# Kernel tuning notes

Hardware: AMD Instinct MI355X
Metric: run time of the kernel (lower is better)

The kernel has to match this reference:

```python
import jax, jax.numpy as jnp
import numpy as np

B, S, H = 2, 2048, 2048
NH, HD = 16, 128


def rotate_half(x):
    x1, x2 = x[..., : x.shape[-1] // 2], x[..., x.shape[-1] // 2 :]
    return jnp.concatenate((-x2, x1), axis=-1)


def setup_inputs() -> dict:
    key = jax.random.key(0)
    ks = jax.random.split(key, 8)
    return {
        "hidden": jax.random.normal(ks[0], (B, S, H), dtype=jnp.float32),
        "cos": jax.random.uniform(ks[1], (S, HD), dtype=jnp.float32),
        "sin": jax.random.uniform(ks[2], (S, HD), dtype=jnp.float32),
        "attention_mask": jnp.zeros((B, 1, S, S), dtype=jnp.float32),
        "Wq": jax.random.normal(ks[3], (H, H), dtype=jnp.float32) * 0.02,
        "Wk": jax.random.normal(ks[4], (H, H), dtype=jnp.float32) * 0.02,
        "Wv": jax.random.normal(ks[5], (H, H), dtype=jnp.float32) * 0.02,
        "Wo": jax.random.normal(ks[6], (H, H), dtype=jnp.float32) * 0.02,
    }


def reference(hidden, cos, sin, attention_mask, Wq, Wk, Wv, Wo):
    b, s, h = hidden.shape
    # torch Linear: y = x @ W.T ; reshape to [B, NH, S, HD]
    def proj(W):
        return (hidden @ W.T).reshape(b, s, NH, HD).transpose(0, 2, 1, 3)

    q, k, v = proj(Wq), proj(Wk), proj(Wv)
    c = cos[None, None, :, :]  # [1,1,S,HD]
    si = sin[None, None, :, :]
    q = q * c + rotate_half(q) * si
    k = k * c + rotate_half(k) * si
    scores = jnp.einsum("bhqd,bhkd->bhqk", q, k) / jnp.sqrt(jnp.float32(HD))
    scores = scores + attention_mask
    attn = jax.nn.softmax(scores.astype(jnp.float32), axis=-1).astype(q.dtype)
    out = jnp.einsum("bhqk,bhkd->bhqd", attn, v)
    out = out.transpose(0, 2, 1, 3).reshape(b, s, h)
    return out @ Wo.T
```

## Files before the change

### kernel.cpp

```cpp
#include <hip/hip_runtime.h>
#include <hip/hip_bf16.h>
#include <math.h>

#define SEQ 2048
#define HID 2048
#define NHEAD 16
#define HDIM 128
#define LDQ 6144

typedef __bf16 bf16_t;
typedef __bf16 bf16x2 __attribute__((ext_vector_type(2)));
typedef __bf16 bf16x4_t __attribute__((ext_vector_type(4)));
typedef __bf16 bf16x8 __attribute__((ext_vector_type(8)));
typedef float f32x4 __attribute__((ext_vector_type(4)));
typedef float f32x16 __attribute__((ext_vector_type(16)));
typedef unsigned u32x4 __attribute__((ext_vector_type(4)));

#define MFMA16(a, b, c) __builtin_amdgcn_mfma_f32_16x16x32_bf16(a, b, c, 0, 0, 0)
#define MFMA32(a, b, c) __builtin_amdgcn_mfma_f32_32x32x16_bf16(a, b, c, 0, 0, 0)
#define GLOAD_LDS(g, l) \
  __builtin_amdgcn_global_load_lds((const __attribute__((address_space(1))) void*)(g), \
                                   (__attribute__((address_space(3))) void*)(l), 16, 0, 0)

static __device__ inline unsigned pk2(float lo, float hi) {
  bf16x2 t; t[0] = (bf16_t)lo; t[1] = (bf16_t)hi;
  return __builtin_bit_cast(unsigned, t);
}

__global__ void cast_hidden(const float* __restrict__ in, bf16_t* __restrict__ out) {
  int i = blockIdx.x * 256 + threadIdx.x;
  float4 v = ((const float4*)in)[i];
  bf16x4_t b;
  b[0] = (bf16_t)v.x; b[1] = (bf16_t)v.y; b[2] = (bf16_t)v.z; b[3] = (bf16_t)v.w;
  ((bf16x4_t*)out)[i] = b;
}

__global__ void cast_weights(const float* __restrict__ a, const float* __restrict__ b,
                             const float* __restrict__ c, const float* __restrict__ d,
                             bf16_t* __restrict__ out) {
  const float* srcs[4] = {a, b, c, d};
  const float* src = srcs[blockIdx.y];
  bf16_t* dst = out + (size_t)blockIdx.y * (HID * HID);
  int i = blockIdx.x * 256 + threadIdx.x;
  float4 v = ((const float4*)src)[i];
  bf16x4_t o;
  o[0] = (bf16_t)v.x; o[1] = (bf16_t)v.y; o[2] = (bf16_t)v.z; o[3] = (bf16_t)v.w;
  ((bf16x4_t*)dst)[i] = o;
}

__global__ __launch_bounds__(512, 2) void gemm256(
    const bf16_t* __restrict__ A, const bf16_t* __restrict__ Bw,
    bf16_t* __restrict__ Cb, float* __restrict__ Cf, int M, int N, int K) {
  __shared__ char smem[131072];
  const int tid = threadIdx.x, lane = tid & 63, wid = tid >> 6;
  const int wr = wid >> 2, wc = wid & 3;
  const int lr = lane & 15, lg = lane >> 4;
  const int xcd = blockIdx.x & 7, l = blockIdx.x >> 3;
  const int brow = (xcd >> 2) * 8 + l / 6;
  const int bcol = (xcd & 3) * 6 + l % 6;
  const int NT = K >> 6;

  const bf16_t* Ab = A + (size_t)(brow * 256) * K;
  const bf16_t* Bb = Bw + (size_t)(bcol * 256) * K;

  f32x4 acc[8][4] = {};
  bf16x8 af[4], bfr[4];
  const int swz = (lg ^ ((lr >> 1) & 3)) << 4;

#define STAGE_HALF(t_, op, kh)                                                        \
  {                                                                                   \
    int tt = (t_) < NT ? (t_) : NT - 1;                                               \
    const bf16_t* gsrc = (op) ? Bb : Ab;                                              \
    char* ldst = smem + (tt & 1) * 65536 + (op) * 32768 + (kh) * 16384;               \
    _Pragma("unroll") for (int is = 0; is < 2; ++is) {                                \
      int p = tid + is * 512;                                                         \
      int row = p >> 2, ch = p & 3;                                                   \
      GLOAD_LDS(gsrc + (size_t)row * K + tt * 64 + (kh) * 32 +                        \
                    ((ch ^ ((row >> 1) & 3)) * 8),                                    \
                ldst + p * 16);                                                       \
    }                                                                                 \
  }

#define PHASE(cb, kh, mh, LOADB, STAGECALL, VM)                                       \
  {                                                                                   \
    _Pragma("unroll") for (int mf = 0; mf < 4; ++mf) {                                \
      int row = wr * 128 + (mh) * 64 + mf * 16 + lr;                                  \
      af[mf] = *(const bf16x8*)(smem + (cb) * 65536 + (kh) * 16384 + row * 64 + swz); \
    }                                                                                 \
    if (LOADB) {                                                                      \
      _Pragma("unroll") for (int nf = 0; nf < 4; ++nf) {                              \
        int row = wc * 64 + nf * 16 + lr;                                             \
        bfr[nf] = *(const bf16x8*)(smem + (cb) * 65536 + 32768 + (kh) * 16384 +       \
                                   row * 64 + swz);                                   \
      }                                                                               \
    }                                                                                 \
    STAGECALL;                                                                        \
    __builtin_amdgcn_s_barrier();                                                     \
    asm volatile("s_waitcnt lgkmcnt(0)" ::: "memory");                                \
    __builtin_amdgcn_sched_barrier(0);                                                \
    __builtin_amdgcn_s_setprio(1);                                                    \
    _Pragma("unroll") for (int mf = 0; mf < 4; ++mf)                                  \
      _Pragma("unroll") for (int nf = 0; nf < 4; ++nf)                                \
        acc[(mh) * 4 + mf][nf] = MFMA16(af[mf], bfr[nf], acc[(mh) * 4 + mf][nf]);     \
    __builtin_amdgcn_s_setprio(0);                                                    \
    if (VM) { asm volatile("s_waitcnt vmcnt(6)" ::: "memory"); }                      \
    __builtin_amdgcn_s_barrier();                                                     \
    __builtin_amdgcn_sched_barrier(0);                                                \
  }

  STAGE_HALF(0, 1, 0); STAGE_HALF(0, 0, 0); STAGE_HALF(0, 1, 1); STAGE_HALF(0, 0, 1);
  STAGE_HALF(1, 1, 0); STAGE_HALF(1, 0, 0); STAGE_HALF(1, 1, 1);
  asm volatile("s_waitcnt vmcnt(6)" ::: "memory");
  __builtin_amdgcn_s_barrier();
  __builtin_amdgcn_sched_barrier(0);

  const int NI = NT >> 1;
  for (int i = 0; i < NI; ++i) {
    const int t2 = 2 * i;
    PHASE(0, 0, 0, 1, STAGE_HALF(t2 + 1, 0, 1), 0);
    PHASE(0, 0, 1, 0, STAGE_HALF(t2 + 2, 1, 0), 0);
    PHASE(0, 1, 0, 1, STAGE_HALF(t2 + 2, 0, 0), 0);
    PHASE(0, 1, 1, 0, STAGE_HALF(t2 + 2, 1, 1), 1);
    PHASE(1, 0, 0, 1, STAGE_HALF(t2 + 2, 0, 1), 0);
    PHASE(1, 0, 1, 0, STAGE_HALF(t2 + 3, 1, 0), 0);
    PHASE(1, 1, 0, 1, STAGE_HALF(t2 + 3, 0, 0), 0);
    PHASE(1, 1, 1, 0, STAGE_HALF(t2 + 3, 1, 1), 1);
  }
#undef PHASE
#undef STAGE_HALF

#pragma unroll
  for (int mi = 0; mi < 8; ++mi)
#pragma unroll
    for (int nf = 0; nf < 4; ++nf)
#pragma unroll
      for (int r = 0; r < 4; ++r) {
        int row = brow * 256 + wr * 128 + (mi >> 2) * 64 + (mi & 3) * 16 + lg * 4 + r;
        int col = bcol * 256 + wc * 64 + nf * 16 + lr;
        float v = acc[mi][nf][r];
        if (Cf) Cf[(size_t)row * N + col] = v;
        else    Cb[(size_t)row * N + col] = (bf16_t)v;
      }
}

__global__ __launch_bounds__(256, 3) void gemm_bt(
    const bf16_t* __restrict__ A, const bf16_t* __restrict__ Bw,
    bf16_t* __restrict__ Cb, float* __restrict__ Cf,
    int M, int N, int K) {
  __shared__ bf16_t As[2][128 * 32];
  __shared__ bf16_t Bs[2][128 * 32];
  const int tid = threadIdx.x;
  const int lane = tid & 63, wid = tid >> 6;
  const int wr = wid >> 1, wc = wid & 1;
  const int lr = lane & 15, lg = lane >> 4;
  const int nwg = gridDim.x;
  const int lid = (blockIdx.x & 7) * (nwg >> 3) + (blockIdx.x >> 3);
  const int nbc = N >> 7;
  const int brow = lid / nbc, bcol = lid % nbc;

  f32x4 acc[4][4] = {};
  const int swz = lg ^ ((lr >> 1) & 3);

  const int srow = tid >> 2, sch = tid & 3;
#define GSTAGE(k0, bb)                                                                   \
  {                                                                                      \
    _Pragma("unroll") for (int is = 0; is < 2; ++is) {                                   \
      int row = srow + is * 64;                                                          \
      int g = (sch ^ ((row >> 1) & 3)) * 8;                                              \
      GLOAD_LDS(A + (size_t)(brow * 128 + row) * K + (k0) + g,                           \
                &As[bb][(row * 4 + sch) * 8]);                                           \
      GLOAD_LDS(Bw + (size_t)(bcol * 128 + row) * K + (k0) + g,                          \
                &Bs[bb][(row * 4 + sch) * 8]);                                           \
    }                                                                                    \
  }

  GSTAGE(0, 0);
  __syncthreads();

  const int nt = K / 32;
  for (int t = 0; t < nt; ++t) {
    const int cb = t & 1;
    if (t + 1 < nt) GSTAGE((t + 1) * 32, cb ^ 1);
    bf16x8 af[4], bfr[4];
#pragma unroll
    for (int m = 0; m < 4; ++m)
      af[m] = *(const bf16x8*)(&As[cb][(wr * 64 + m * 16 + lr) * 32 + swz * 8]);
#pragma unroll
    for (int n = 0; n < 4; ++n)
      bfr[n] = *(const bf16x8*)(&Bs[cb][(wc * 64 + n * 16 + lr) * 32 + swz * 8]);
#pragma unroll
    for (int m = 0; m < 4; ++m)
#pragma unroll
      for (int n = 0; n < 4; ++n)
        acc[m][n] = MFMA16(af[m], bfr[n], acc[m][n]);
    __syncthreads();
  }
#undef GSTAGE

#pragma unroll
  for (int m = 0; m < 4; ++m)
#pragma unroll
    for (int n = 0; n < 4; ++n)
#pragma unroll
      for (int r = 0; r < 4; ++r) {
        int row = brow * 128 + wr * 64 + m * 16 + lg * 4 + r;
        int col = bcol * 128 + wc * 64 + n * 16 + lr;
        float v = acc[m][n][r];
        if (Cf) Cf[(size_t)row * N + col] = v;
        else    Cb[(size_t)row * N + col] = (bf16_t)v;
      }
}

__global__ void rope_qk(bf16_t* __restrict__ QKV,
                        const float* __restrict__ cost, const float* __restrict__ sint) {
  const float SCALE = 0.08838834764831845f;
  int idx = blockIdx.x * 256 + threadIdx.x;
  int d8 = idx & 7;
  int t = idx >> 3;
  int h = t & 15;
  int row = t >> 4;
  int s = row & (SEQ - 1);
  size_t base = (size_t)row * LDQ + h * HDIM;
  const float4* cp = (const float4*)(cost + s * HDIM);
  const float4* sp = (const float4*)(sint + s * HDIM);
  float4 c0a = cp[d8 * 2], c0b = cp[d8 * 2 + 1];
  float4 c1a = cp[16 + d8 * 2], c1b = cp[16 + d8 * 2 + 1];
  float4 s0a = sp[d8 * 2], s0b = sp[d8 * 2 + 1];
  float4 s1a = sp[16 + d8 * 2], s1b = sp[16 + d8 * 2 + 1];
  float c0[8] = {c0a.x, c0a.y, c0a.z, c0a.w, c0b.x, c0b.y, c0b.z, c0b.w};
  float c1[8] = {c1a.x, c1a.y, c1a.z, c1a.w, c1b.x, c1b.y, c1b.z, c1b.w};
  float s0[8] = {s0a.x, s0a.y, s0a.z, s0a.w, s0b.x, s0b.y, s0b.z, s0b.w};
  float s1[8] = {s1a.x, s1a.y, s1a.z, s1a.w, s1b.x, s1b.y, s1b.z, s1b.w};

  bf16_t* Q = QKV;
  bf16_t* K = QKV + 2048;
  bf16x8 qlo = *(bf16x8*)(Q + base + d8 * 8);
  bf16x8 qhi = *(bf16x8*)(Q + base + 64 + d8 * 8);
  bf16x8 klo = *(bf16x8*)(K + base + d8 * 8);
  bf16x8 khi = *(bf16x8*)(K + base + 64 + d8 * 8);
  bf16x8 qlo2, qhi2, klo2, khi2;
#pragma unroll
  for (int j = 0; j < 8; ++j) {
    float q0 = (float)qlo[j], q1 = (float)qhi[j];
    qlo2[j] = (bf16_t)((q0 * c0[j] - q1 * s0[j]) * SCALE);
    qhi2[j] = (bf16_t)((q1 * c1[j] + q0 * s1[j]) * SCALE);
    float k0 = (float)klo[j], k1 = (float)khi[j];
    klo2[j] = (bf16_t)(k0 * c0[j] - k1 * s0[j]);
    khi2[j] = (bf16_t)(k1 * c1[j] + k0 * s1[j]);
  }
  *(bf16x8*)(Q + base + d8 * 8) = qlo2;
  *(bf16x8*)(Q + base + 64 + d8 * 8) = qhi2;
  *(bf16x8*)(K + base + d8 * 8) = klo2;
  *(bf16x8*)(K + base + 64 + d8 * 8) = khi2;
}

__global__ void transpose_v(const bf16_t* __restrict__ Vf, bf16_t* __restrict__ Vt) {
  __shared__ bf16_t t[32][33];
  int tx = threadIdx.x & 31, ty = threadIdx.x >> 5;
  int r0 = blockIdx.y * 32, c0 = blockIdx.x * 32;
#pragma unroll
  for (int j = 0; j < 4; ++j)
    t[ty + j * 8][tx] = Vf[(size_t)(r0 + ty + j * 8) * LDQ + c0 + tx];
  __syncthreads();
#pragma unroll
  for (int j = 0; j < 4; ++j) {
    int c = c0 + ty + j * 8;
    int r = r0 + tx;
    int h = c >> 7, d = c & 127, b = r >> 11, s = r & (SEQ - 1);
    Vt[(((size_t)(b * NHEAD + h)) * HDIM + d) * SEQ + s] = t[tx][ty + j * 8];
  }
}

__global__ __launch_bounds__(512, 2) void flash_fwd(
    const bf16_t* __restrict__ Qf, const bf16_t* __restrict__ Kf,
    const bf16_t* __restrict__ Vt, const float* __restrict__ mask,
    bf16_t* __restrict__ AO) {
  __shared__ char smem[131072];
  char* KsB = smem;
  char* VsB = smem + 65536;
  const int tid = threadIdx.x, lane = tid & 63, wid = tid >> 6;
  const int q32 = lane & 31, hi = lane >> 5;

  const int x = blockIdx.x;
  const int bh = x & 31, qt = x >> 5;
  const int b = bh >> 4, h = bh & 15;
  const int qg = qt * 256 + wid * 32 + q32;

  bf16x8 qf[8];
  const bf16_t* qptr = Qf + (size_t)(b * SEQ + qg) * LDQ + h * HDIM + hi * 8;
#pragma unroll
  for (int ds = 0; ds < 8; ++ds) qf[ds] = *(const bf16x8*)(qptr + ds * 16);

  const float* mp = mask + (size_t)b * SEQ * SEQ + (size_t)qg * SEQ + hi * 4;

  float mrun = -INFINITY, lpart = 0.f;
  f32x16 o[4] = {};

#define STAGE_KV(kt_, bb)                                                                \
  {                                                                                      \
    const int kb0_ = (kt_) * 128;                                                        \
    _Pragma("unroll") for (int is = 0; is < 4; ++is) {                                   \
      int p = tid + is * 512;                                                            \
      int row = p >> 4, ch = p & 15;                                                     \
      int src = (ch * 16) ^ ((row & 7) << 4);                                            \
      GLOAD_LDS((const char*)(Kf + (size_t)(b * SEQ + kb0_ + row) * LDQ + h * HDIM) +    \
                    src,                                                                 \
                KsB + (bb) * 32768 + p * 16);                                            \
      GLOAD_LDS((const char*)(Vt + (size_t)(bh * HDIM + row) * SEQ + kb0_) + src,        \
                VsB + (bb) * 32768 + p * 16);                                            \
    }                                                                                    \
  }

  STAGE_KV(0, 0);
  __syncthreads();

  const int NT = SEQ / 128;
  for (int kt = 0; kt < NT; ++kt) {
    const int cur = kt & 1;
    const int kb0 = kt * 128;
    if (kt + 1 < NT) STAGE_KV(kt + 1, cur ^ 1);

#pragma unroll
    for (int kb = 0; kb < 4; ++kb) {
      f32x16 sacc;
#pragma unroll
      for (int g = 0; g < 4; ++g) {
        float4 m4 = *(const float4*)(mp + kb0 + kb * 32 + 8 * g);
        sacc[4 * g + 0] = m4.x; sacc[4 * g + 1] = m4.y;
        sacc[4 * g + 2] = m4.z; sacc[4 * g + 3] = m4.w;
      }
#pragma unroll
      for (int ds = 0; ds < 8; ++ds) {
        int row = kb * 32 + q32;
        bf16x8 kfr = *(const bf16x8*)(KsB + cur * 32768 + row * 256 +
                                      ((ds * 32 + hi * 16) ^ ((row & 7) << 4)));
        sacc = MFMA32(kfr, qf[ds], sacc);
      }

      float mx = sacc[0];
#pragma unroll
      for (int r = 1; r < 16; ++r) mx = fmaxf(mx, sacc[r]);
      mx = fmaxf(mx, __shfl_xor(mx, 32, 64));
      if (!__all(mx <= mrun + 8.f)) {
        float mnew = fmaxf(mrun, mx);
        float corr = __expf(mrun - mnew);
        mrun = mnew;
        lpart *= corr;
#pragma unroll
        for (int d0 = 0; d0 < 4; ++d0)
#pragma unroll
          for (int r = 0; r < 16; ++r) o[d0][r] *= corr;
      }

      float p[16];
      float rs = 0.f;
#pragma unroll
      for (int r = 0; r < 16; ++r) {
        p[r] = __expf(sacc[r] - mrun);
        rs += p[r];
      }
      lpart += rs;

#pragma unroll
      for (int s = 0; s < 2; ++s) {
        unsigned A1 = pk2(p[8 * s + 0], p[8 * s + 1]);
        unsigned A2 = pk2(p[8 * s + 2], p[8 * s + 3]);
        unsigned B1 = pk2(p[8 * s + 4], p[8 * s + 5]);
        unsigned B2 = pk2(p[8 * s + 6], p[8 * s + 7]);
        unsigned A1s = __shfl_xor(A1, 32, 64);
        unsigned A2s = __shfl_xor(A2, 32, 64);
        unsigned B1s = __shfl_xor(B1, 32, 64);
        unsigned B2s = __shfl_xor(B2, 32, 64);
        unsigned w0 = hi ? B1s : A1;
        unsigned w1 = hi ? B2s : A2;
        unsigned w2 = hi ? B1 : A1s;
        unsigned w3 = hi ? B2 : A2s;
        u32x4 W = {w0, w1, w2, w3};
        bf16x8 pav = __builtin_bit_cast(bf16x8, W);
        const int gs = kb * 2 + s;
#pragma unroll
        for (int d0 = 0; d0 < 4; ++d0) {
          int vrow = d0 * 32 + q32;
          bf16x8 vf = *(const bf16x8*)(VsB + cur * 32768 + vrow * 256 +
                                       ((gs * 32 + hi * 16) ^ ((vrow & 7) << 4)));
          o[d0] = MFMA32(vf, pav, o[d0]);
        }
      }
    }
    __syncthreads();
  }
#undef STAGE_KV

  float l = lpart + __shfl_xor(lpart, 32, 64);
  float rl = 1.f / l;
  bf16_t* aorow = AO + (size_t)(b * SEQ + qg) * HID + h * HDIM;
#pragma unroll
  for (int d0 = 0; d0 < 4; ++d0)
#pragma unroll
    for (int g = 0; g < 4; ++g) {
      unsigned lo = pk2(o[d0][4 * g + 0] * rl, o[d0][4 * g + 1] * rl);
      unsigned hi2 = pk2(o[d0][4 * g + 2] * rl, o[d0][4 * g + 3] * rl);
      int d = d0 * 32 + 8 * g + 4 * hi;
      *(unsigned*)(aorow + d) = lo;
      *(unsigned*)(aorow + d + 2) = hi2;
    }
}

extern "C" void kernel_launch(void* const* d_in, const int* in_sizes, int n_in,
                              void* d_out, int out_size, void* d_ws, size_t ws_size,
                              hipStream_t stream) {
  const float* hidden = (const float*)d_in[0];
  const float* cost   = (const float*)d_in[1];
  const float* sint   = (const float*)d_in[2];
  const float* mask   = (const float*)d_in[3];
  const float* Wq     = (const float*)d_in[4];
  const float* Wk     = (const float*)d_in[5];
  const float* Wv     = (const float*)d_in[6];
  const float* Wo     = (const float*)d_in[7];
  float* out = (float*)d_out;
  char* ws = (char*)d_ws;

  bf16_t* Af  = (bf16_t*)(ws + 0);
  bf16_t* Wqb = (bf16_t*)(ws + 16777216);
  bf16_t* Wob = (bf16_t*)(ws + 41943040);
  bf16_t* QKV = (bf16_t*)(ws + 50331648);
  bf16_t* Vt  = (bf16_t*)(ws + 0);
  bf16_t* AO  = (bf16_t*)(ws + 16777216);

  cast_hidden<<<8192, 256, 0, stream>>>(hidden, Af);
  cast_weights<<<dim3(4096, 4), 256, 0, stream>>>(Wq, Wk, Wv, Wo, Wqb);

  gemm256<<<384, 512, 0, stream>>>(Af, Wqb, QKV, nullptr, 4096, LDQ, HID);

  rope_qk<<<2048, 256, 0, stream>>>(QKV, cost, sint);
  transpose_v<<<dim3(64, 128), 256, 0, stream>>>(QKV + 4096, Vt);

  flash_fwd<<<256, 512, 0, stream>>>(QKV, QKV + 2048, Vt, mask, AO);

  gemm_bt<<<512, 256, 0, stream>>>(AO, Wob, nullptr, out, 4096, HID, HID);
}
```

Before: 312.9 us.

## Split QKV GEMM into QK and V GEMMs, pre-transpose mask to bf16

The fused QKV projection becomes a 256-block GEMM for Q and K only (ld 4096), with V computed by a separate gemm_bt launch. A new kernel transposes the attention mask and converts it to bf16, so flash_fwd reads it key-major with per-element scalar loads instead of float4 rows. This adds an extra launch plus a full mask transpose pass, and changes mask precision to bf16. The scalar strided mask loads in the inner loop could cost more than the float4 reads they replace.

```diff
diff --git a/kernel.cpp b/kernel.cpp
--- a/kernel.cpp
+++ b/kernel.cpp
@@ -6,7 +6,7 @@
 #define HID 2048
 #define NHEAD 16
 #define HDIM 128
-#define LDQ 6144
+#define LDK 4096
 
 typedef __bf16 bf16_t;
 typedef __bf16 bf16x2 __attribute__((ext_vector_type(2)));
@@ -56,8 +56,8 @@
   const int wr = wid >> 2, wc = wid & 3;
   const int lr = lane & 15, lg = lane >> 4;
   const int xcd = blockIdx.x & 7, l = blockIdx.x >> 3;
-  const int brow = (xcd >> 2) * 8 + l / 6;
-  const int bcol = (xcd & 3) * 6 + l % 6;
+  const int brow = (xcd >> 2) * 8 + (l >> 2);
+  const int bcol = (xcd & 3) * 4 + (l & 3);
   const int NT = K >> 6;
 
   const bf16_t* Ab = A + (size_t)(brow * 256) * K;
@@ -211,7 +211,7 @@
       }
 }
 
-__global__ void rope_qk(bf16_t* __restrict__ QKV,
+__global__ void rope_qk(bf16_t* __restrict__ QK,
                         const float* __restrict__ cost, const float* __restrict__ sint) {
   const float SCALE = 0.08838834764831845f;
   int idx = blockIdx.x * 256 + threadIdx.x;
@@ -220,7 +220,7 @@
   int h = t & 15;
   int row = t >> 4;
   int s = row & (SEQ - 1);
-  size_t base = (size_t)row * LDQ + h * HDIM;
+  size_t base = (size_t)row * LDK + h * HDIM;
   const float4* cp = (const float4*)(cost + s * HDIM);
   const float4* sp = (const float4*)(sint + s * HDIM);
   float4 c0a = cp[d8 * 2], c0b = cp[d8 * 2 + 1];
@@ -232,8 +232,8 @@
   float s0[8] = {s0a.x, s0a.y, s0a.z, s0a.w, s0b.x, s0b.y, s0b.z, s0b.w};
   float s1[8] = {s1a.x, s1a.y, s1a.z, s1a.w, s1b.x, s1b.y, s1b.z, s1b.w};
 
-  bf16_t* Q = QKV;
-  bf16_t* K = QKV + 2048;
+  bf16_t* Q = QK;
+  bf16_t* K = QK + 2048;
   bf16x8 qlo = *(bf16x8*)(Q + base + d8 * 8);
   bf16x8 qhi = *(bf16x8*)(Q + base + 64 + d8 * 8);
   bf16x8 klo = *(bf16x8*)(K + base + d8 * 8);
@@ -260,7 +260,7 @@
   int r0 = blockIdx.y * 32, c0 = blockIdx.x * 32;
 #pragma unroll
   for (int j = 0; j < 4; ++j)
-    t[ty + j * 8][tx] = Vf[(size_t)(r0 + ty + j * 8) * LDQ + c0 + tx];
+    t[ty + j * 8][tx] = Vf[(size_t)(r0 + ty + j * 8) * HID + c0 + tx];
   __syncthreads();
 #pragma unroll
   for (int j = 0; j < 4; ++j) {
@@ -271,9 +271,24 @@
   }
 }
 
+__global__ void mask_t(const float* __restrict__ m, bf16_t* __restrict__ mt) {
+  __shared__ float t[32][33];
+  int tx = threadIdx.x & 31, ty = threadIdx.x >> 5;
+  int r0 = blockIdx.y * 32, c0 = blockIdx.x * 32;
+  const float* mb = m + (size_t)blockIdx.z * SEQ * SEQ;
+  bf16_t* mtb = mt + (size_t)blockIdx.z * SEQ * SEQ;
+#pragma unroll
+  for (int j = 0; j < 4; ++j)
+    t[ty + j * 8][tx] = mb[(size_t)(r0 + ty + j * 8) * SEQ + c0 + tx];
+  __syncthreads();
+#pragma unroll
+  for (int j = 0; j < 4; ++j)
+    mtb[(size_t)(c0 + ty + j * 8) * SEQ + r0 + tx] = (bf16_t)t[tx][ty + j * 8];
+}
+
 __global__ __launch_bounds__(512, 2) void flash_fwd(
     const bf16_t* __restrict__ Qf, const bf16_t* __restrict__ Kf,
-    const bf16_t* __restrict__ Vt, const float* __restrict__ mask,
+    const bf16_t* __restrict__ Vt, const bf16_t* __restrict__ maskT,
     bf16_t* __restrict__ AO) {
   __shared__ char smem[131072];
   char* KsB = smem;
@@ -287,11 +302,11 @@
   const int qg = qt * 256 + wid * 32 + q32;
 
   bf16x8 qf[8];
-  const bf16_t* qptr = Qf + (size_t)(b * SEQ + qg) * LDQ + h * HDIM + hi * 8;
+  const bf16_t* qptr = Qf + (size_t)(b * SEQ + qg) * LDK + h * HDIM + hi * 8;
 #pragma unroll
   for (int ds = 0; ds < 8; ++ds) qf[ds] = *(const bf16x8*)(qptr + ds * 16);
 
-  const float* mp = mask + (size_t)b * SEQ * SEQ + (size_t)qg * SEQ + hi * 4;
+  const bf16_t* mQ = maskT + (size_t)b * SEQ * SEQ + qg;
 
   float mrun = -INFINITY, lpart = 0.f;
   f32x16 o[4] = {};
@@ -303,7 +318,7 @@
       int p = tid + is * 512;                                                            \
       int row = p >> 4, ch = p & 15;                                                     \
       int src = (ch * 16) ^ ((row & 7) << 4);                                            \
-      GLOAD_LDS((const char*)(Kf + (size_t)(b * SEQ + kb0_ + row) * LDQ + h * HDIM) +    \
+      GLOAD_LDS((const char*)(Kf + (size_t)(b * SEQ + kb0_ + row) * LDK + h * HDIM) +    \
                     src,                                                                 \
                 KsB + (bb) * 32768 + p * 16);                                            \
       GLOAD_LDS((const char*)(Vt + (size_t)(bh * HDIM + row) * SEQ + kb0_) + src,        \
@@ -324,10 +339,9 @@
     for (int kb = 0; kb < 4; ++kb) {
       f32x16 sacc;
 #pragma unroll
-      for (int g = 0; g < 4; ++g) {
-        float4 m4 = *(const float4*)(mp + kb0 + kb * 32 + 8 * g);
-        sacc[4 * g + 0] = m4.x; sacc[4 * g + 1] = m4.y;
-        sacc[4 * g + 2] = m4.z; sacc[4 * g + 3] = m4.w;
+      for (int r = 0; r < 16; ++r) {
+        int key = kb0 + kb * 32 + (r & 3) + 8 * (r >> 2) + 4 * hi;
+        sacc[r] = (float)mQ[(size_t)key * SEQ];
       }
 #pragma unroll
       for (int ds = 0; ds < 8; ++ds) {
@@ -420,22 +434,27 @@
   float* out = (float*)d_out;
   char* ws = (char*)d_ws;
 
-  bf16_t* Af  = (bf16_t*)(ws + 0);
-  bf16_t* Wqb = (bf16_t*)(ws + 16777216);
-  bf16_t* Wob = (bf16_t*)(ws + 41943040);
-  bf16_t* QKV = (bf16_t*)(ws + 50331648);
-  bf16_t* Vt  = (bf16_t*)(ws + 0);
-  bf16_t* AO  = (bf16_t*)(ws + 16777216);
+  bf16_t* Af    = (bf16_t*)(ws + 0);
+  bf16_t* Wqb   = (bf16_t*)(ws + 16777216);
+  bf16_t* Wvb   = (bf16_t*)(ws + 33554432);
+  bf16_t* Wob   = (bf16_t*)(ws + 41943040);
+  bf16_t* QK    = (bf16_t*)(ws + 50331648);
+  bf16_t* Vf    = (bf16_t*)(ws + 83886080);
+  bf16_t* Vt    = (bf16_t*)(ws + 0);
+  bf16_t* maskT = (bf16_t*)(ws + 83886080);
+  bf16_t* AO    = (bf16_t*)(ws + 16777216);
 
   cast_hidden<<<8192, 256, 0, stream>>>(hidden, Af);
   cast_weights<<<dim3(4096, 4), 256, 0, stream>>>(Wq, Wk, Wv, Wo, Wqb);
 
-  gemm256<<<384, 512, 0, stream>>>(Af, Wqb, QKV, nullptr, 4096, LDQ, HID);
-
-  rope_qk<<<2048, 256, 0, stream>>>(QKV, cost, sint);
-  transpose_v<<<dim3(64, 128), 256, 0, stream>>>(QKV + 4096, Vt);
-
-  flash_fwd<<<256, 512, 0, stream>>>(QKV, QKV + 2048, Vt, mask, AO);
+  gemm256<<<256, 512, 0, stream>>>(Af, Wqb, QK, nullptr, 4096, LDK, HID);
+  gemm_bt<<<512, 256, 0, stream>>>(Af, Wvb, Vf, nullptr, 4096, HID, HID);
+
+  rope_qk<<<2048, 256, 0, stream>>>(QK, cost, sint);
+  transpose_v<<<dim3(64, 128), 256, 0, stream>>>(Vf, Vt);
+  mask_t<<<dim3(64, 64, 2), 256, 0, stream>>>(mask, maskT);
+
+  flash_fwd<<<256, 512, 0, stream>>>(QK, QK + 2048, Vt, maskT, AO);
 
   gemm_bt<<<512, 256, 0, stream>>>(AO, Wob, nullptr, out, 4096, HID, HID);
 }
```

After: 319.0 us. About the same (+1.9%).
